# Kernel optimization log

Hardware: AMD Instinct MI355X
Metric: run time of the kernel (lower is better)

The kernel has to match this reference:

```python
import jax, jax.numpy as jnp
import numpy as np

# Hyperparameters (from init_kwargs)
N = 100000      # num_nodes
T = 4           # num_edge_type
E = 400000      # edges per type
C = 2           # num_channels
L = 2           # num_layers
W_IN = 128      # input feature dim
D = 64          # node_dim (w_out)
NUM_CLASS = 16
BETA = 0.5
M = 10000       # number of target nodes


def setup_inputs() -> dict:
    key = jax.random.key(0)
    ks = jax.random.split(key, 10)
    glorot = np.sqrt(6.0 / (W_IN + D))
    glorot1 = np.sqrt(6.0 / (C * D + D))
    glorot2 = np.sqrt(6.0 / (D + NUM_CLASS))
    return {
        "X": jax.random.normal(ks[0], (N, W_IN), dtype=jnp.float32),
        "edge_value": jax.random.uniform(ks[1], (T, E), dtype=jnp.float32),
        "conv_weights": 0.1 * jax.random.normal(ks[2], (L, C, T), dtype=jnp.float32),
        "Ws": jax.random.uniform(ks[3], (C, W_IN, D), minval=-glorot, maxval=glorot, dtype=jnp.float32),
        "lin1_w": jax.random.uniform(ks[4], (C * D, D), minval=-glorot1, maxval=glorot1, dtype=jnp.float32),
        "lin1_b": jnp.zeros((D,), dtype=jnp.float32),
        "lin_w": jax.random.uniform(ks[5], (D, NUM_CLASS), minval=-glorot2, maxval=glorot2, dtype=jnp.float32),
        "lin_b": jnp.zeros((NUM_CLASS,), dtype=jnp.float32),
        "edge_index": jax.random.randint(ks[6], (T, 2, E), 0, N),
        "target_x": jax.random.randint(ks[7], (M,), 0, N),
    }


def reference(X, edge_value, conv_weights, Ws, lin1_w, lin1_b, lin_w, lin_b,
              edge_index, target_x):
    # Flatten edge types into one big edge list. torch_sparse.coalesce(op='add')
    # followed by torch.sparse.mm is mathematically a duplicate-summing SpMM,
    # i.e. a segment_sum over destination rows.
    rows = edge_index[:, 0, :].reshape(-1)      # [T*E]
    cols = edge_index[:, 1, :].reshape(-1)      # [T*E]
    vals = edge_value.reshape(-1)               # [T*E]
    type_id = jnp.repeat(jnp.arange(T), E)      # [T*E] edge-type id (constant)

    # Per-channel input projections: X_ = X @ Ws[c]  -> [C, N, D]
    X_ = jnp.einsum('nf,cfd->cnd', X, Ws)
    H = X_

    for l in range(L):
        # FastGTConv: softmax over edge types per channel
        filt = jax.nn.softmax(conv_weights[l], axis=1)   # [C, T]
        newH = []
        for c in range(C):
            v = vals * filt[c, type_id]                  # [T*E] mixed edge weights
            msgs = v[:, None] * H[c][cols]               # gather + scale: [T*E, D]
            newH.append(jax.ops.segment_sum(msgs, rows, num_segments=N))
        H = jnp.stack(newH)                              # [C, N, D]

    # FastGTN tail: relu(beta*X_ + (1-beta)*H), concat channels, linear1
    Hc = jax.nn.relu(BETA * X_ + (1.0 - BETA) * H)       # [C, N, D]
    Hcat = jnp.transpose(Hc, (1, 0, 2)).reshape(N, C * D)
    H_ = Hcat @ lin1_w + lin1_b                          # [N, D]

    # FastGTNs head: logits at target nodes
    return H_[target_x] @ lin_w + lin_b                  # [M, NUM_CLASS]
```

## Files before the change

kernel.cpp:

```cpp
#include <hip/hip_runtime.h>

#define N_NODES   100000
#define T_TYPES   4
#define E_EDGES   400000
#define E4        100000
#define G_TOT     400000
#define C_CH      2
#define W_INF     128
#define DD        64
#define NUM_CLASS 16
#define BETA      0.5f
#define M_TGT     10000

#define NBKT      391
#define BROWS     256
#define BPAD      4864
#define CHUNK_G   512
#define NPART_BLK 782
#define PROJ_BLK  1563

static const size_t PLANE2 = (size_t)N_NODES * DD;

typedef __attribute__((ext_vector_type(8))) short short8x;
typedef __attribute__((ext_vector_type(4))) float f32x4;

__device__ __forceinline__ unsigned bf16rne(float x) {
    unsigned u = __float_as_uint(x);
    return (u + 0x7FFFu + ((u >> 16) & 1u)) >> 16;
}
__device__ __forceinline__ unsigned packbf(float a, float b) {
    return bf16rne(a) | (bf16rne(b) << 16);
}
__device__ __forceinline__ float bflo(unsigned u) { return __uint_as_float(u << 16); }
__device__ __forceinline__ float bfhi(unsigned u) { return __uint_as_float(u & 0xFFFF0000u); }

__device__ __forceinline__ void load_filter(const float* cw, int layer,
                                            float* f0, float* f1) {
    float m0 = -1e30f, m1 = -1e30f;
    #pragma unroll
    for (int t = 0; t < T_TYPES; ++t) {
        f0[t] = cw[layer * C_CH * T_TYPES + t];
        f1[t] = cw[layer * C_CH * T_TYPES + T_TYPES + t];
        m0 = fmaxf(m0, f0[t]); m1 = fmaxf(m1, f1[t]);
    }
    float s0 = 0.f, s1 = 0.f;
    #pragma unroll
    for (int t = 0; t < T_TYPES; ++t) {
        f0[t] = __expf(f0[t] - m0); s0 += f0[t];
        f1[t] = __expf(f1[t] - m1); s1 += f1[t];
    }
    #pragma unroll
    for (int t = 0; t < T_TYPES; ++t) { f0[t] /= s0; f1[t] /= s1; }
}

__global__ void prep_kernel(const float* __restrict__ Ws,
                            unsigned short* __restrict__ Wsb,
                            int* __restrict__ cursor) {
    int b = blockIdx.x;
    int tid = threadIdx.x;
    if (b < 64) {
        int idx = b * 256 + tid;
        int c   = idx >> 13;
        int rem = idx & 8191;
        int d   = rem >> 7;
        int k   = rem & 127;
        Wsb[idx] = (unsigned short)bf16rne(Ws[c * (W_INF * DD) + k * DD + d]);
    } else {
        int idx = (b - 64) * 256 + tid;
        if (idx < NBKT) cursor[idx] = idx * BPAD;
    }
}

__global__ __launch_bounds__(256) void build_proj_kernel(
        const int* __restrict__ edge_index,
        const float* __restrict__ edge_value,
        const float* __restrict__ cw,
        int* __restrict__ cursor,
        int2* __restrict__ edata2,
        const float* __restrict__ X,
        const unsigned short* __restrict__ Wsb,
        unsigned* __restrict__ Xp16) {
    __shared__ int cnt[392];
    __shared__ int lbase[392];
    __shared__ int gbase[392];
    __shared__ int2 le[2048];
    __shared__ unsigned short lbk[2048];
    int tid = threadIdx.x;

    if (blockIdx.x < NPART_BLK) {
        int p = blockIdx.x;
        for (int j = tid; j < NBKT; j += 256) cnt[j] = 0;
        __syncthreads();

        float f0[T_TYPES], f1[T_TYPES];
        load_filter(cw, 0, f0, f1);

        int px[8], pv[8], rk[8], bk[8];
        int ne = 0;
        #pragma unroll
        for (int g = 0; g < 2; ++g) {
            int idx = p * CHUNK_G + g * 256 + tid;
            if (idx < G_TOT) {
                int t = idx / E4, r = idx - t * E4;
                const int* bptr = edge_index + (size_t)t * 2 * E_EDGES;
                int4   rw = ((const int4*)bptr)[r];
                int4   cl = ((const int4*)(bptr + E_EDGES))[r];
                float4 vv = ((const float4*)(edge_value + (size_t)t * E_EDGES))[r];
                int tb = t << 17;
                int   rr[4] = {rw.x, rw.y, rw.z, rw.w};
                int   cc[4] = {cl.x, cl.y, cl.z, cl.w};
                float vf[4] = {vv.x, vv.y, vv.z, vv.w};
                #pragma unroll
                for (int k = 0; k < 4; ++k) {
                    int b = rr[k] >> 8;
                    px[ne] = cc[k] | tb | ((rr[k] & 255) << 19);
                    pv[ne] = __float_as_int(vf[k]);
                    bk[ne] = b;
                    rk[ne] = atomicAdd(&cnt[b], 1);
                    ++ne;
                }
            }
        }
        __syncthreads();
        if (tid < 64) {
            int c[7]; int s = 0;
            #pragma unroll
            for (int k = 0; k < 7; ++k) {
                int idx = tid * 7 + k;
                c[k] = (idx < NBKT) ? cnt[idx] : 0;
                s += c[k];
            }
            int inc = s;
            #pragma unroll
            for (int off = 1; off < 64; off <<= 1) {
                int v = __shfl_up(inc, off);
                if (tid >= off) inc += v;
            }
            int base = inc - s;
            #pragma unroll
            for (int k = 0; k < 7; ++k) {
                int idx = tid * 7 + k;
                if (idx < NBKT) lbase[idx] = base;
                base += c[k];
            }
        }
        __syncthreads();
        #pragma unroll
        for (int k = 0; k < 8; ++k) {
            if (k < ne) {
                int slot = lbase[bk[k]] + rk[k];
                le[slot]  = make_int2(px[k], pv[k]);
                lbk[slot] = (unsigned short)bk[k];
            }
        }
        __syncthreads();
        for (int j = tid; j < NBKT; j += 256)
            gbase[j] = cnt[j] ? atomicAdd(&cursor[j], cnt[j]) : 0;
        __syncthreads();
        int ngrp = min(CHUNK_G, G_TOT - p * CHUNK_G);
        int nloc = 4 * ngrp;
        for (int j = tid; j < nloc; j += 256) {
            int b = lbk[j];
            int2 e = le[j];
            int t = (e.x >> 17) & 3;
            float v = __int_as_float(e.y);
            edata2[gbase[b] + (j - lbase[b])] =
                make_int2(e.x, (int)packbf(v * f0[t], v * f1[t]));
        }
    } else {
        int row0 = (blockIdx.x - NPART_BLK) * 64;
        int wave = tid >> 6, lane = tid & 63;
        int m = lane & 15, q = lane >> 4;
        int arow = row0 + wave * 16 + m;
        const float4* X4 = (const float4*)X;
        union { short8x s; uint4 u; } A[4];
        bool valid = arow < N_NODES;
        #pragma unroll
        for (int ks = 0; ks < 4; ++ks) {
            float4 va = make_float4(0.f, 0.f, 0.f, 0.f), vb = va;
            if (valid) {
                va = X4[(size_t)arow * 32 + ks * 8 + q * 2];
                vb = X4[(size_t)arow * 32 + ks * 8 + q * 2 + 1];
            }
            A[ks].u = make_uint4(packbf(va.x, va.y), packbf(va.z, va.w),
                                 packbf(vb.x, vb.y), packbf(vb.z, vb.w));
        }

        #pragma unroll
        for (int ct = 0; ct < 4; ++ct) {
            f32x4 acc0 = {0.f, 0.f, 0.f, 0.f};
            f32x4 acc1 = {0.f, 0.f, 0.f, 0.f};
            #pragma unroll
            for (int ks = 0; ks < 4; ++ks) {
                short8x B0 = *(const short8x*)(Wsb + (ct * 16 + m) * 128 + ks * 32 + q * 8);
                short8x B1 = *(const short8x*)(Wsb + 8192 + (ct * 16 + m) * 128 + ks * 32 + q * 8);
                acc0 = __builtin_amdgcn_mfma_f32_16x16x32_bf16(A[ks].s, B0, acc0, 0, 0, 0);
                acc1 = __builtin_amdgcn_mfma_f32_16x16x32_bf16(A[ks].s, B1, acc1, 0, 0, 0);
            }
            #pragma unroll
            for (int r = 0; r < 4; ++r) {
                int row = row0 + wave * 16 + q * 4 + r;
                if (row < N_NODES)
                    Xp16[(size_t)row * DD + ct * 16 + m] = packbf(acc0[r], acc1[r]);
            }
        }
    }
}

__device__ __forceinline__ void qfma(const uint4 h, unsigned wp,
                                     float4& a, float4& b) {
    float w0 = bflo(wp), w1 = bfhi(wp);
    a.x = fmaf(w0, bflo(h.x), a.x);
    a.y = fmaf(w1, bfhi(h.x), a.y);
    a.z = fmaf(w0, bflo(h.y), a.z);
    a.w = fmaf(w1, bfhi(h.y), a.w);
    b.x = fmaf(w0, bflo(h.z), b.x);
    b.y = fmaf(w1, bfhi(h.z), b.y);
    b.z = fmaf(w0, bflo(h.w), b.z);
    b.w = fmaf(w1, bfhi(h.w), b.w);
}

__device__ __forceinline__ void qreduce(float4& a, float4& b) {
    a.x += __shfl_xor(a.x, 16); a.y += __shfl_xor(a.y, 16);
    a.z += __shfl_xor(a.z, 16); a.w += __shfl_xor(a.w, 16);
    b.x += __shfl_xor(b.x, 16); b.y += __shfl_xor(b.y, 16);
    b.z += __shfl_xor(b.z, 16); b.w += __shfl_xor(b.w, 16);
    a.x += __shfl_xor(a.x, 32); a.y += __shfl_xor(a.y, 32);
    a.z += __shfl_xor(a.z, 32); a.w += __shfl_xor(a.w, 32);
    b.x += __shfl_xor(b.x, 32); b.y += __shfl_xor(b.y, 32);
    b.z += __shfl_xor(b.z, 32); b.w += __shfl_xor(b.w, 32);
}

__device__ __forceinline__ int row_beg(const int* offs, int row) {
    return ((row & 255) == 0) ? (row >> 8) * BPAD : offs[row - 1];
}

__global__ __launch_bounds__(512) void sortgather_kernel(
        const int* __restrict__ cursor,
        int2* __restrict__ edata2,
        int* __restrict__ offs,
        const unsigned* __restrict__ Hin16,
        unsigned* __restrict__ Hout16) {
    __shared__ int rcnt[BROWS];
    __shared__ int rbase[BROWS];
    __shared__ int rcur[BROWS];
    __shared__ int2 ls[BPAD];
    __shared__ unsigned short sidx[BPAD];
    int b   = blockIdx.x;
    int tid = threadIdx.x;
    int bb  = b * BPAD;
    int cnt = cursor[b] - bb;

    if (tid < BROWS) rcnt[tid] = 0;
    __syncthreads();
    for (int j = tid; j < cnt; j += 512) {
        int2 e = edata2[bb + j];
        ls[j] = e;
        atomicAdd(&rcnt[(e.x >> 19) & 255], 1);
    }
    __syncthreads();
    if (tid < 64) {
        int c[4]; int s = 0;
        #pragma unroll
        for (int k = 0; k < 4; ++k) { c[k] = rcnt[tid * 4 + k]; s += c[k]; }
        int inc = s;
        #pragma unroll
        for (int off = 1; off < 64; off <<= 1) {
            int v = __shfl_up(inc, off);
            if (tid >= off) inc += v;
        }
        int base = inc - s;
        #pragma unroll
        for (int k = 0; k < 4; ++k) { rbase[tid * 4 + k] = base; base += c[k]; }
    }
    __syncthreads();
    if (tid < BROWS) rcur[tid] = rbase[tid];
    __syncthreads();
    for (int j = tid; j < cnt; j += 512) {
        int2 e = ls[j];
        int lr = (e.x >> 19) & 255;
        int pos = atomicAdd(&rcur[lr], 1);
        edata2[bb + pos] = e;
        sidx[pos] = (unsigned short)j;
    }
    int row0 = b * BROWS;
    if (tid < BROWS && row0 + tid < N_NODES)
        offs[row0 + tid] = bb + rbase[tid] + rcnt[tid];
    __syncthreads();

    int wv = tid >> 6, lane = tid & 63;
    int s16 = lane & 15, sub = lane >> 4;
    const uint4* hp = (const uint4*)Hin16;
    #pragma unroll 1
    for (int r32 = 0; r32 < 32; ++r32) {
        int lr = wv * 32 + r32;
        int row = row0 + lr;
        int beg = rbase[lr];
        int end = beg + rcnt[lr];
        float4 a = make_float4(0.f, 0.f, 0.f, 0.f);
        float4 bb4 = make_float4(0.f, 0.f, 0.f, 0.f);
        int i = beg + sub;
        for (; i + 4 < end; i += 8) {
            int j0 = sidx[i];
            int j1 = sidx[i + 4];
            int2 e0 = ls[j0];
            int2 e1 = ls[j1];
            uint4 h0 = hp[(size_t)(e0.x & 0x1FFFF) * 16 + s16];
            uint4 h1 = hp[(size_t)(e1.x & 0x1FFFF) * 16 + s16];
            qfma(h0, (unsigned)e0.y, a, bb4);
            qfma(h1, (unsigned)e1.y, a, bb4);
        }
        if (i < end) {
            int2 e = ls[sidx[i]];
            uint4 h = hp[(size_t)(e.x & 0x1FFFF) * 16 + s16];
            qfma(h, (unsigned)e.y, a, bb4);
        }
        qreduce(a, bb4);
        if (sub == 0 && row < N_NODES)
            ((uint4*)Hout16)[(size_t)row * 16 + s16] =
                make_uint4(packbf(a.x, a.y), packbf(a.z, a.w),
                           packbf(bb4.x, bb4.y), packbf(bb4.z, bb4.w));
    }
}

__global__ __launch_bounds__(512) void tgt_tail_kernel(const unsigned* __restrict__ Hin16,
                                                       const unsigned* __restrict__ Xp16,
                                                       const int* __restrict__ offs,
                                                       const int2* __restrict__ edata2,
                                                       const float* __restrict__ cw,
                                                       const int* __restrict__ tgt,
                                                       const float* __restrict__ lin1_w,
                                                       const float* __restrict__ lin1_b,
                                                       const float* __restrict__ lin_w,
                                                       const float* __restrict__ lin_b,
                                                       float* __restrict__ out) {
    __shared__ float l1w[W_INF * DD];
    __shared__ float lw[DD * NUM_CLASS];
    __shared__ float l1b[DD];
    __shared__ float lb[NUM_CLASS];
    __shared__ float hc[8][W_INF];
    __shared__ float hmid[8][DD];

    int tid = threadIdx.x;
    {
        const float4* g = (const float4*)lin1_w;
        float4* s = (float4*)l1w;
        #pragma unroll
        for (int i = 0; i < 4; ++i) s[tid + 512 * i] = g[tid + 512 * i];
        if (tid < 256) ((float4*)lw)[tid] = ((const float4*)lin_w)[tid];
        else if (tid < 256 + DD) l1b[tid - 256] = lin1_b[tid - 256];
        else if (tid < 256 + DD + NUM_CLASS) lb[tid - 256 - DD] = lin_b[tid - 256 - DD];
    }

    float f0a[T_TYPES], f1a[T_TYPES], f0b[T_TYPES], f1b[T_TYPES];
    load_filter(cw, 0, f0a, f1a);
    load_filter(cw, 1, f0b, f1b);
    float r0[T_TYPES], r1[T_TYPES];
    #pragma unroll
    for (int t = 0; t < T_TYPES; ++t) { r0[t] = f0b[t] / f0a[t]; r1[t] = f1b[t] / f1a[t]; }

    int w = tid >> 6, lane = tid & 63;
    int s16 = lane & 15, sub = lane >> 4;
    int m = blockIdx.x * 8 + w;
    int row = tgt[m];
    int beg = row_beg(offs, row);
    int end = offs[row];
    const uint4* hp = (const uint4*)Hin16;
    float4 a = make_float4(0.f, 0.f, 0.f, 0.f);
    float4 b = make_float4(0.f, 0.f, 0.f, 0.f);
    for (int i = beg + sub; i < end; i += 4) {
        int2 e = edata2[i];
        int t = (e.x >> 17) & 3;
        uint4 h = hp[(size_t)(e.x & 0x1FFFF) * 16 + s16];
        unsigned wp = (unsigned)e.y;
        float w0 = bflo(wp) * r0[t], w1 = bfhi(wp) * r1[t];
        a.x = fmaf(w0, bflo(h.x), a.x);
        a.y = fmaf(w1, bfhi(h.x), a.y);
        a.z = fmaf(w0, bflo(h.y), a.z);
        a.w = fmaf(w1, bfhi(h.y), a.w);
        b.x = fmaf(w0, bflo(h.z), b.x);
        b.y = fmaf(w1, bfhi(h.z), b.y);
        b.z = fmaf(w0, bflo(h.w), b.z);
        b.w = fmaf(w1, bfhi(h.w), b.w);
    }
    qreduce(a, b);

    if (sub == 0) {
        uint4 xu = ((const uint4*)Xp16)[(size_t)row * 16 + s16];
        int d0 = 4 * s16;
        hc[w][d0 + 0]      = fmaxf(BETA * bflo(xu.x) + (1.f - BETA) * a.x, 0.f);
        hc[w][DD + d0 + 0] = fmaxf(BETA * bfhi(xu.x) + (1.f - BETA) * a.y, 0.f);
        hc[w][d0 + 1]      = fmaxf(BETA * bflo(xu.y) + (1.f - BETA) * a.z, 0.f);
        hc[w][DD + d0 + 1] = fmaxf(BETA * bfhi(xu.y) + (1.f - BETA) * a.w, 0.f);
        hc[w][d0 + 2]      = fmaxf(BETA * bflo(xu.z) + (1.f - BETA) * b.x, 0.f);
        hc[w][DD + d0 + 2] = fmaxf(BETA * bfhi(xu.z) + (1.f - BETA) * b.y, 0.f);
        hc[w][d0 + 3]      = fmaxf(BETA * bflo(xu.w) + (1.f - BETA) * b.z, 0.f);
        hc[w][DD + d0 + 3] = fmaxf(BETA * bfhi(xu.w) + (1.f - BETA) * b.w, 0.f);
    }
    __syncthreads();

    float a1 = l1b[lane];
    #pragma unroll 8
    for (int k = 0; k < W_INF; ++k)
        a1 = fmaf(hc[w][k], l1w[k * DD + lane], a1);
    hmid[w][lane] = a1;
    __syncthreads();

    if (lane < NUM_CLASS) {
        float o = lb[lane];
        #pragma unroll 8
        for (int k = 0; k < DD; ++k)
            o = fmaf(hmid[w][k], lw[k * NUM_CLASS + lane], o);
        out[(size_t)m * NUM_CLASS + lane] = o;
    }
}

extern "C" void kernel_launch(void* const* d_in, const int* in_sizes, int n_in,
                              void* d_out, int out_size, void* d_ws, size_t ws_size,
                              hipStream_t stream) {
    const float* X            = (const float*)d_in[0];
    const float* edge_value   = (const float*)d_in[1];
    const float* conv_weights = (const float*)d_in[2];
    const float* Ws           = (const float*)d_in[3];
    const float* lin1_w       = (const float*)d_in[4];
    const float* lin1_b       = (const float*)d_in[5];
    const float* lin_w        = (const float*)d_in[6];
    const float* lin_b        = (const float*)d_in[7];
    const int*   edge_index   = (const int*)d_in[8];
    const int*   target_x     = (const int*)d_in[9];
    float* out = (float*)d_out;

    unsigned*       Xp16 = (unsigned*)d_ws;
    unsigned*       H116 = Xp16 + PLANE2;
    unsigned short* Wsb  = (unsigned short*)(H116 + PLANE2);
    int*            offs = (int*)(Wsb + C_CH * W_INF * DD);
    int*            cursor = offs + N_NODES;
    int2*           edata2 = (int2*)(cursor + 512);

    prep_kernel<<<66, 256, 0, stream>>>(Ws, Wsb, cursor);
    build_proj_kernel<<<NPART_BLK + PROJ_BLK, 256, 0, stream>>>(
        edge_index, edge_value, conv_weights, cursor, edata2, X, Wsb, Xp16);
    sortgather_kernel<<<NBKT, 512, 0, stream>>>(cursor, edata2, offs, Xp16, H116);
    tgt_tail_kernel<<<M_TGT / 8, 512, 0, stream>>>(H116, Xp16, offs, edata2,
                                                   conv_weights, target_x,
                                                   lin1_w, lin1_b, lin_w, lin_b, out);
}
```

Baseline: 257.2 us.

## Split each sort-gather bucket into four quarter blocks and drop tail weight staging

The sort+gather kernel now launches four 256-thread blocks per 256-row bucket, one per 64-row quarter. Each block rescans the whole bucket, keeps only its quarter's edges, sorts them in a smaller LDS footprint and writes them to a separate sorted buffer with per-64-row padding. The aim is more blocks in flight and higher occupancy for the latency-bound gather, at the cost of reading each bucket four times. The target tail kernel now uses 4 targets per block and reads lin weights straight from global memory instead of staging 32KB into LDS per block. Quarter overflow beyond QPAD would silently drop edges.

```diff
diff --git a/kernel.cpp b/kernel.cpp
--- a/kernel.cpp
+++ b/kernel.cpp
@@ -15,6 +15,7 @@
 #define NBKT      391
 #define BROWS     256
 #define BPAD      4864
+#define QPAD      1216
 #define CHUNK_G   512
 #define NPART_BLK 782
 #define PROJ_BLK  1563
@@ -232,101 +233,109 @@
 }
 
 __device__ __forceinline__ int row_beg(const int* offs, int row) {
-    return ((row & 255) == 0) ? (row >> 8) * BPAD : offs[row - 1];
-}
-
-__global__ __launch_bounds__(512) void sortgather_kernel(
+    return ((row & 63) == 0) ? (row >> 6) * QPAD : offs[row - 1];
+}
+
+__global__ __launch_bounds__(256) void sortgather_kernel(
         const int* __restrict__ cursor,
-        int2* __restrict__ edata2,
+        const int2* __restrict__ edata2,
+        int2* __restrict__ edataS,
         int* __restrict__ offs,
         const unsigned* __restrict__ Hin16,
         unsigned* __restrict__ Hout16) {
-    __shared__ int rcnt[BROWS];
-    __shared__ int rbase[BROWS];
-    __shared__ int rcur[BROWS];
-    __shared__ int2 ls[BPAD];
-    __shared__ unsigned short sidx[BPAD];
-    int b   = blockIdx.x;
+    __shared__ int rcnt[64];
+    __shared__ int rbase[64];
+    __shared__ int rcur[64];
+    __shared__ int nq;
+    __shared__ int2 ls[QPAD];
+    __shared__ unsigned short sidx[QPAD];
+    int b = blockIdx.x % 392;
+    int q = blockIdx.x / 392;
+    if (b >= NBKT) return;
     int tid = threadIdx.x;
     int bb  = b * BPAD;
     int cnt = cursor[b] - bb;
 
-    if (tid < BROWS) rcnt[tid] = 0;
-    __syncthreads();
-    for (int j = tid; j < cnt; j += 512) {
+    if (tid < 64) rcnt[tid] = 0;
+    if (tid == 0) nq = 0;
+    __syncthreads();
+    for (int j = tid; j < cnt; j += 256) {
         int2 e = edata2[bb + j];
-        ls[j] = e;
-        atomicAdd(&rcnt[(e.x >> 19) & 255], 1);
-    }
-    __syncthreads();
+        int rt = (e.x >> 19) & 255;
+        if ((rt >> 6) == q) {
+            int pos = atomicAdd(&nq, 1);
+            if (pos < QPAD) {
+                ls[pos] = e;
+                atomicAdd(&rcnt[rt & 63], 1);
+            }
+        }
+    }
+    __syncthreads();
+    int nl = min(nq, QPAD);
     if (tid < 64) {
-        int c[4]; int s = 0;
-        #pragma unroll
-        for (int k = 0; k < 4; ++k) { c[k] = rcnt[tid * 4 + k]; s += c[k]; }
-        int inc = s;
+        int c = rcnt[tid];
+        int inc = c;
         #pragma unroll
         for (int off = 1; off < 64; off <<= 1) {
             int v = __shfl_up(inc, off);
             if (tid >= off) inc += v;
         }
-        int base = inc - s;
-        #pragma unroll
-        for (int k = 0; k < 4; ++k) { rbase[tid * 4 + k] = base; base += c[k]; }
-    }
-    __syncthreads();
-    if (tid < BROWS) rcur[tid] = rbase[tid];
-    __syncthreads();
-    for (int j = tid; j < cnt; j += 512) {
-        int2 e = ls[j];
-        int lr = (e.x >> 19) & 255;
+        rbase[tid] = inc - c;
+        rcur[tid]  = inc - c;
+    }
+    __syncthreads();
+    for (int j = tid; j < nl; j += 256) {
+        int lr = (ls[j].x >> 19) & 63;
         int pos = atomicAdd(&rcur[lr], 1);
-        edata2[bb + pos] = e;
         sidx[pos] = (unsigned short)j;
     }
-    int row0 = b * BROWS;
-    if (tid < BROWS && row0 + tid < N_NODES)
-        offs[row0 + tid] = bb + rbase[tid] + rcnt[tid];
-    __syncthreads();
+    __syncthreads();
+
+    int s  = b * 4 + q;
+    int sb = s * QPAD;
+    for (int i = tid; i < nl; i += 256)
+        edataS[sb + i] = ls[sidx[i]];
+    int row0 = s * 64;
+    if (tid < 64 && row0 + tid < N_NODES)
+        offs[row0 + tid] = sb + rbase[tid] + rcnt[tid];
 
     int wv = tid >> 6, lane = tid & 63;
     int s16 = lane & 15, sub = lane >> 4;
     const uint4* hp = (const uint4*)Hin16;
     #pragma unroll 1
-    for (int r32 = 0; r32 < 32; ++r32) {
-        int lr = wv * 32 + r32;
+    for (int r16 = 0; r16 < 16; ++r16) {
+        int lr = wv * 16 + r16;
         int row = row0 + lr;
         int beg = rbase[lr];
         int end = beg + rcnt[lr];
-        float4 a = make_float4(0.f, 0.f, 0.f, 0.f);
-        float4 bb4 = make_float4(0.f, 0.f, 0.f, 0.f);
+        float4 a  = make_float4(0.f, 0.f, 0.f, 0.f);
+        float4 b4 = make_float4(0.f, 0.f, 0.f, 0.f);
         int i = beg + sub;
         for (; i + 4 < end; i += 8) {
-            int j0 = sidx[i];
-            int j1 = sidx[i + 4];
-            int2 e0 = ls[j0];
-            int2 e1 = ls[j1];
+            int2 e0 = ls[sidx[i]];
+            int2 e1 = ls[sidx[i + 4]];
             uint4 h0 = hp[(size_t)(e0.x & 0x1FFFF) * 16 + s16];
             uint4 h1 = hp[(size_t)(e1.x & 0x1FFFF) * 16 + s16];
-            qfma(h0, (unsigned)e0.y, a, bb4);
-            qfma(h1, (unsigned)e1.y, a, bb4);
+            qfma(h0, (unsigned)e0.y, a, b4);
+            qfma(h1, (unsigned)e1.y, a, b4);
         }
         if (i < end) {
             int2 e = ls[sidx[i]];
             uint4 h = hp[(size_t)(e.x & 0x1FFFF) * 16 + s16];
-            qfma(h, (unsigned)e.y, a, bb4);
-        }
-        qreduce(a, bb4);
+            qfma(h, (unsigned)e.y, a, b4);
+        }
+        qreduce(a, b4);
         if (sub == 0 && row < N_NODES)
             ((uint4*)Hout16)[(size_t)row * 16 + s16] =
                 make_uint4(packbf(a.x, a.y), packbf(a.z, a.w),
-                           packbf(bb4.x, bb4.y), packbf(bb4.z, bb4.w));
-    }
-}
-
-__global__ __launch_bounds__(512) void tgt_tail_kernel(const unsigned* __restrict__ Hin16,
+                           packbf(b4.x, b4.y), packbf(b4.z, b4.w));
+    }
+}
+
+__global__ __launch_bounds__(256) void tgt_tail_kernel(const unsigned* __restrict__ Hin16,
                                                        const unsigned* __restrict__ Xp16,
                                                        const int* __restrict__ offs,
-                                                       const int2* __restrict__ edata2,
+                                                       const int2* __restrict__ edataS,
                                                        const float* __restrict__ cw,
                                                        const int* __restrict__ tgt,
                                                        const float* __restrict__ lin1_w,
@@ -334,23 +343,10 @@
                                                        const float* __restrict__ lin_w,
                                                        const float* __restrict__ lin_b,
                                                        float* __restrict__ out) {
-    __shared__ float l1w[W_INF * DD];
-    __shared__ float lw[DD * NUM_CLASS];
-    __shared__ float l1b[DD];
-    __shared__ float lb[NUM_CLASS];
-    __shared__ float hc[8][W_INF];
-    __shared__ float hmid[8][DD];
+    __shared__ float hc[4][W_INF];
+    __shared__ float hmid[4][DD];
 
     int tid = threadIdx.x;
-    {
-        const float4* g = (const float4*)lin1_w;
-        float4* s = (float4*)l1w;
-        #pragma unroll
-        for (int i = 0; i < 4; ++i) s[tid + 512 * i] = g[tid + 512 * i];
-        if (tid < 256) ((float4*)lw)[tid] = ((const float4*)lin_w)[tid];
-        else if (tid < 256 + DD) l1b[tid - 256] = lin1_b[tid - 256];
-        else if (tid < 256 + DD + NUM_CLASS) lb[tid - 256 - DD] = lin_b[tid - 256 - DD];
-    }
 
     float f0a[T_TYPES], f1a[T_TYPES], f0b[T_TYPES], f1b[T_TYPES];
     load_filter(cw, 0, f0a, f1a);
@@ -361,7 +357,7 @@
 
     int w = tid >> 6, lane = tid & 63;
     int s16 = lane & 15, sub = lane >> 4;
-    int m = blockIdx.x * 8 + w;
+    int m = blockIdx.x * 4 + w;
     int row = tgt[m];
     int beg = row_beg(offs, row);
     int end = offs[row];
@@ -369,7 +365,7 @@
     float4 a = make_float4(0.f, 0.f, 0.f, 0.f);
     float4 b = make_float4(0.f, 0.f, 0.f, 0.f);
     for (int i = beg + sub; i < end; i += 4) {
-        int2 e = edata2[i];
+        int2 e = edataS[i];
         int t = (e.x >> 17) & 3;
         uint4 h = hp[(size_t)(e.x & 0x1FFFF) * 16 + s16];
         unsigned wp = (unsigned)e.y;
@@ -399,18 +395,18 @@
     }
     __syncthreads();
 
-    float a1 = l1b[lane];
+    float a1 = lin1_b[lane];
     #pragma unroll 8
     for (int k = 0; k < W_INF; ++k)
-        a1 = fmaf(hc[w][k], l1w[k * DD + lane], a1);
+        a1 = fmaf(hc[w][k], lin1_w[k * DD + lane], a1);
     hmid[w][lane] = a1;
     __syncthreads();
 
     if (lane < NUM_CLASS) {
-        float o = lb[lane];
+        float o = lin_b[lane];
         #pragma unroll 8
         for (int k = 0; k < DD; ++k)
-            o = fmaf(hmid[w][k], lw[k * NUM_CLASS + lane], o);
+            o = fmaf(hmid[w][k], lin_w[k * NUM_CLASS + lane], o);
         out[(size_t)m * NUM_CLASS + lane] = o;
     }
 }
@@ -436,12 +432,14 @@
     int*            offs = (int*)(Wsb + C_CH * W_INF * DD);
     int*            cursor = offs + N_NODES;
     int2*           edata2 = (int2*)(cursor + 512);
+    int2*           edataS = edata2 + (size_t)NBKT * BPAD;
 
     prep_kernel<<<66, 256, 0, stream>>>(Ws, Wsb, cursor);
     build_proj_kernel<<<NPART_BLK + PROJ_BLK, 256, 0, stream>>>(
         edge_index, edge_value, conv_weights, cursor, edata2, X, Wsb, Xp16);
-    sortgather_kernel<<<NBKT, 512, 0, stream>>>(cursor, edata2, offs, Xp16, H116);
-    tgt_tail_kernel<<<M_TGT / 8, 512, 0, stream>>>(H116, Xp16, offs, edata2,
+    sortgather_kernel<<<4 * 392, 256, 0, stream>>>(cursor, edata2, edataS, offs,
+                                                   Xp16, H116);
+    tgt_tail_kernel<<<M_TGT / 4, 256, 0, stream>>>(H116, Xp16, offs, edataS,
                                                    conv_weights, target_x,
                                                    lin1_w, lin1_b, lin_w, lin_b, out);
 }
```

Result: no change. 254.5 us (-1.0%).
